# Kernel tuning notes

Hardware: AMD Instinct MI355X
Metric: run time of the kernel (lower is better)

Reference implementation:

```python
import jax, jax.numpy as jnp
import numpy as np

N, E, F_IN, H = 50000, 800000, 500, 96

def setup_inputs() -> dict:
    key = jax.random.key(0)
    ks = jax.random.split(key, 10)
    x = jax.random.normal(ks[0], (N, F_IN), dtype=jnp.float32)
    src = jax.random.randint(ks[1], (E,), 0, N, dtype=jnp.int32)
    dst = jax.random.randint(ks[2], (E,), 0, N, dtype=jnp.int32)
    perm = jax.random.permutation(ks[3], N).astype(jnp.int32)
    W1 = jax.random.normal(ks[4], (F_IN, H), dtype=jnp.float32) / np.sqrt(F_IN)
    b1 = jnp.zeros((H,), jnp.float32)
    a1 = jnp.full((H,), 0.25, jnp.float32)  # PReLU init
    W2 = jax.random.normal(ks[5], (H, H), dtype=jnp.float32) / np.sqrt(H)
    b2 = jnp.zeros((H,), jnp.float32)
    a2 = jnp.full((H,), 0.25, jnp.float32)
    Wm = jax.random.normal(ks[6], (H, H), dtype=jnp.float32) / np.sqrt(H)
    bm = jnp.zeros((H,), jnp.float32)
    return {"x": x, "src": src, "dst": dst, "perm": perm,
            "W1": W1, "b1": b1, "a1": a1, "W2": W2, "b2": b2, "a2": a2,
            "Wm": Wm, "bm": bm}

def reference(x, src, dst, perm, W1, b1, a1, W2, b2, a2, Wm, bm):
    n = x.shape[0]
    ones = jnp.ones_like(src, dtype=x.dtype)
    deg_out = jnp.clip(jax.ops.segment_sum(ones, src, num_segments=n), 1.0)
    deg_in = jnp.clip(jax.ops.segment_sum(ones, dst, num_segments=n), 1.0)
    norm_out = (deg_out ** -0.5)[:, None]  # [N,1]
    norm_in = (deg_in ** -0.5)[:, None]

    def gconv(h, W, b, a):
        # DGL GraphConv, norm='both': D_out^-1/2 -> W -> A -> D_in^-1/2 -> +b -> PReLU
        h = (h * norm_out) @ W                                  # [N,H]
        agg = jax.ops.segment_sum(h[src], dst, num_segments=n)  # SpMM via gather/scatter
        h = agg * norm_in + b
        return jnp.where(h >= 0, h, a * h)                      # PReLU

    def encode(feat):
        h = gconv(feat, W1, b1, a1)
        return gconv(h, W2, b2, a2)

    z1 = encode(x)
    z2 = encode(x[perm])  # corrupted view: permuted node features
    z1 = z1 @ Wm + bm
    z2 = z2 @ Wm + bm
    return jnp.concatenate([z1.sum(1), z2.sum(1)], axis=0)  # [2N]
```

## Files before the change

### kernel.cpp

```cpp
#include <hip/hip_runtime.h>

#define H96 96

typedef __attribute__((ext_vector_type(8))) short bf16x8_t;
typedef __attribute__((ext_vector_type(4))) float f32x4_t;
typedef __attribute__((ext_vector_type(8))) _Float16 half8_t;

__global__ void deg8_kernel(const int* __restrict__ src, const int* __restrict__ dst,
                            int* __restrict__ d8, int E, int NP8) {
    int e = blockIdx.x * blockDim.x + threadIdx.x;
    int c = blockIdx.x & 7;
    if (e < E) {
        int* base = d8 + (size_t)c * 2 * NP8;
        atomicAdd(base + src[e], 1);
        atomicAdd(base + NP8 + dst[e], 1);
    }
}

__global__ void degred_kernel(const int* __restrict__ d8, const int* __restrict__ perm,
                              int* __restrict__ deg_in, int* __restrict__ iperm,
                              float* __restrict__ no, float* __restrict__ ni,
                              int N, int NP8) {
    int i = blockIdx.x * 256 + threadIdx.x;
    if (i >= N) return;
    int so = 0, si = 0;
#pragma unroll
    for (int c = 0; c < 8; c++) {
        so += d8[(size_t)c * 2 * NP8 + i];
        si += d8[(size_t)c * 2 * NP8 + NP8 + i];
    }
    deg_in[i] = si;
    no[i] = rsqrtf(fmaxf((float)so, 1.0f));
    ni[i] = rsqrtf(fmaxf((float)si, 1.0f));
    iperm[perm[i]] = i;
}

__global__ void scanA_kernel(const int* __restrict__ in, int* __restrict__ pre,
                             int* __restrict__ bsums, int n) {
    __shared__ int s[256];
    int i = blockIdx.x * 256 + threadIdx.x;
    int v = (i < n) ? in[i] : 0;
    s[threadIdx.x] = v;
    __syncthreads();
    for (int off = 1; off < 256; off <<= 1) {
        int t = (threadIdx.x >= off) ? s[threadIdx.x - off] : 0;
        __syncthreads();
        s[threadIdx.x] += t;
        __syncthreads();
    }
    if (i < n) pre[i] = s[threadIdx.x] - v;
    if (threadIdx.x == 255) bsums[blockIdx.x] = s[255];
}

__global__ void scanB_kernel(int* __restrict__ bsums, int nb) {
    __shared__ int s[256];
    int v = (threadIdx.x < nb) ? bsums[threadIdx.x] : 0;
    s[threadIdx.x] = v;
    __syncthreads();
    for (int off = 1; off < 256; off <<= 1) {
        int t = (threadIdx.x >= off) ? s[threadIdx.x - off] : 0;
        __syncthreads();
        s[threadIdx.x] += t;
        __syncthreads();
    }
    if (threadIdx.x < nb) bsums[threadIdx.x] = s[threadIdx.x] - v;
}

__global__ void rowfin_kernel(const int* __restrict__ pre, const int* __restrict__ bsums,
                              int* __restrict__ row_start, int* __restrict__ cursor,
                              int N, int E) {
    int i = blockIdx.x * 256 + threadIdx.x;
    if (i < N) {
        int v = pre[i] + bsums[blockIdx.x];
        row_start[i] = v;
        cursor[i] = v;
    }
    if (i == 0) row_start[N] = E;
}

__global__ void scatter_kernel(const int* __restrict__ src, const int* __restrict__ dst,
                               const float* __restrict__ norm_out,
                               int* __restrict__ cursor, int2* __restrict__ edge2, int E) {
    int e = blockIdx.x * 256 + threadIdx.x;
    if (e < E) {
        int d = dst[e];
        int s = src[e];
        int p = atomicAdd(cursor + d, 1);
        edge2[p] = make_int2(s, __float_as_int(norm_out[s]));
    }
}

__global__ void histblk_kernel(const int* __restrict__ deg, int* __restrict__ hb,
                               int N, int nb) {
    __shared__ int h[256];
    h[threadIdx.x] = 0;
    __syncthreads();
    int i = blockIdx.x * 256 + threadIdx.x;
    if (i < N) atomicAdd(&h[min(deg[i], 255)], 1);
    __syncthreads();
    hb[threadIdx.x * nb + blockIdx.x] = h[threadIdx.x];
}

__global__ void place2_kernel(const int* __restrict__ deg, const int* __restrict__ hpre,
                              const int* __restrict__ bsums, int* __restrict__ order,
                              int N, int nb) {
    __shared__ int cur[256];
    int idx = threadIdx.x * nb + blockIdx.x;
    cur[threadIdx.x] = hpre[idx] + bsums[idx >> 8];
    __syncthreads();
    int i = blockIdx.x * 256 + threadIdx.x;
    if (i < N) {
        int b = min(deg[i], 255);
        int p = atomicAdd(&cur[b], 1);
        order[p] = i;
    }
}

__device__ __forceinline__ void f2bf2(float v, unsigned short& h, unsigned short& l) {
    unsigned int b = __float_as_uint(v);
    unsigned short hh = (unsigned short)((b + 0x7FFFu + ((b >> 16) & 1u)) >> 16);
    float fh = __uint_as_float(((unsigned int)hh) << 16);
    float r = v - fh;
    unsigned int rb = __float_as_uint(r);
    unsigned short ll = (unsigned short)((rb + 0x7FFFu + ((rb >> 16) & 1u)) >> 16);
    h = hh; l = ll;
}

__device__ __forceinline__ void cvt8(const float f[8], bf16x8_t& ah, bf16x8_t& al) {
    union { unsigned int u[4]; bf16x8_t v; } H, L;
#pragma unroll
    for (int i = 0; i < 4; i++) {
        float v0 = f[2 * i], v1 = f[2 * i + 1];
        unsigned int b0 = __float_as_uint(v0);
        unsigned int b1 = __float_as_uint(v1);
        unsigned int m0 = b0 & 0xFFFF0000u;
        unsigned int m1 = b1 & 0xFFFF0000u;
        float r0 = v0 - __uint_as_float(m0);
        float r1 = v1 - __uint_as_float(m1);
        H.u[i] = (b0 >> 16) | m1;
        L.u[i] = (__float_as_uint(r0) >> 16) | (__float_as_uint(r1) & 0xFFFF0000u);
    }
    ah = H.v; al = L.v;
}

__global__ void weights_prep(const float* __restrict__ W1, const float* __restrict__ W2,
                             const float* __restrict__ Wm, const float* __restrict__ bm,
                             unsigned short* __restrict__ w1h, unsigned short* __restrict__ w1l,
                             unsigned short* __restrict__ w2h, unsigned short* __restrict__ w2l,
                             float* __restrict__ wsum, float* __restrict__ bsum,
                             int F, int KP1) {
    int idx = blockIdx.x * 256 + threadIdx.x;
    int z1 = 96 * KP1, z2 = z1 + 96 * 96;
    if (idx < z1) {
        int n = idx / KP1, k = idx - n * KP1;
        float v = (k < F) ? W1[(size_t)k * 96 + n] : 0.f;
        unsigned short h, l;
        f2bf2(v, h, l);
        w1h[idx] = h; w1l[idx] = l;
    } else if (idx < z2) {
        int t = idx - z1;
        int n = t / 96, k = t - n * 96;
        float v = W2[(size_t)k * 96 + n];
        unsigned short h, l;
        f2bf2(v, h, l);
        w2h[t] = h; w2l[t] = l;
    } else if (idx < z2 + 96) {
        int c = idx - z2;
        float s = 0.f;
        for (int j = 0; j < 96; j++) s += Wm[c * 96 + j];
        wsum[c] = s;
    } else if (idx == z2 + 96) {
        float s = 0.f;
        for (int j = 0; j < 96; j++) s += bm[j];
        bsum[0] = s;
    }
}

#define GBM 64
#define GBK 32

__device__ __forceinline__ void gload_lds16(const void* g, void* l) {
    __builtin_amdgcn_global_load_lds(
        (const __attribute__((address_space(1))) unsigned int*)g,
        (__attribute__((address_space(3))) unsigned int*)l, 16, 0, 0);
}

__global__ __launch_bounds__(256, 6) void gemm_mfma(const void* __restrict__ Av,
                                                    const unsigned short* __restrict__ Bth,
                                                    const unsigned short* __restrict__ Btl,
                                                    _Float16* __restrict__ C16,
                                                    const int* __restrict__ ipermArr,
                                                    int M, int K, int KP) {
    __shared__ alignas(16) unsigned short Bs[2][2][96][4][8];
    int tid = threadIdx.x;
    int wid = tid >> 6, lane = tid & 63;
    int q = lane >> 4, mn = lane & 15;
    int row0 = blockIdx.x * GBM + wid * 16;
    int arow = min(row0 + mn, M - 1);
    int nk = (K + GBK - 1) / GBK;

    const float* A32 = (const float*)Av;

    const unsigned short* gsrc[3];
    int lbase[3];
#pragma unroll
    for (int i = 0; i < 3; i++) {
        int c = wid * 192 + i * 64 + lane;
        int part = (c >= 384) ? 1 : 0;
        int rem = c - part * 384;
        int row = rem >> 2, slot = rem & 3;
        int kc = slot ^ ((row >> 1) & 3);
        gsrc[i] = (part ? Btl : Bth) + (size_t)row * KP + kc * 8;
        lbase[i] = (wid * 192 + i * 64) * 8;
    }

    auto stage = [&](int t, int buf) {
#pragma unroll
        for (int i = 0; i < 3; i++)
            gload_lds16(gsrc[i] + (size_t)t * GBK, &Bs[buf][0][0][0][0] + lbase[i]);
    };

    auto loadA = [&](int t, float* f) {
        int gk = t * GBK + q * 8;
        if (gk + 8 <= K) {
            float4 v0 = *(const float4*)(A32 + (size_t)arow * K + gk);
            float4 v1 = *(const float4*)(A32 + (size_t)arow * K + gk + 4);
            f[0] = v0.x; f[1] = v0.y; f[2] = v0.z; f[3] = v0.w;
            f[4] = v1.x; f[5] = v1.y; f[6] = v1.z; f[7] = v1.w;
        } else {
#pragma unroll
            for (int c = 0; c < 8; c++)
                f[c] = (gk + c < K) ? A32[(size_t)arow * K + gk + c] : 0.f;
        }
    };

    f32x4_t acc[6] = {};
    float f[8], fn[8];

    stage(0, 0);
    loadA(0, f);

    int slotR = q ^ ((mn >> 1) & 3);

    for (int t = 0; t < nk; t++) {
        int tn = (t + 1 < nk) ? t + 1 : nk - 1;
        stage(tn, (t + 1) & 1);
        loadA(tn, fn);
        asm volatile("s_waitcnt vmcnt(5)" ::: "memory");
        __builtin_amdgcn_sched_barrier(0);
        __builtin_amdgcn_s_barrier();

        bf16x8_t ah, al;
        cvt8(f, ah, al);

        const unsigned short* bp = &Bs[t & 1][0][0][0][0] + mn * 32 + slotR * 8;
#pragma unroll
        for (int ct = 0; ct < 6; ct++) {
            bf16x8_t bh = *(const bf16x8_t*)(bp + ct * 512);
            bf16x8_t bl = *(const bf16x8_t*)(bp + 3072 + ct * 512);
            acc[ct] = __builtin_amdgcn_mfma_f32_16x16x32_bf16(ah, bh, acc[ct], 0, 0, 0);
            acc[ct] = __builtin_amdgcn_mfma_f32_16x16x32_bf16(ah, bl, acc[ct], 0, 0, 0);
            acc[ct] = __builtin_amdgcn_mfma_f32_16x16x32_bf16(al, bh, acc[ct], 0, 0, 0);
        }
        asm volatile("s_waitcnt lgkmcnt(0)" ::: "memory");
        __builtin_amdgcn_sched_barrier(0);
        __builtin_amdgcn_s_barrier();

#pragma unroll
        for (int c = 0; c < 8; c++) f[c] = fn[c];
    }

    asm volatile("s_waitcnt vmcnt(0)" ::: "memory");
    __builtin_amdgcn_sched_barrier(0);

#pragma unroll
    for (int reg = 0; reg < 4; reg++) {
        int gr = row0 + q * 4 + reg;
        if (gr < M) {
            int ip = ipermArr[gr];
#pragma unroll
            for (int ct = 0; ct < 6; ct++) {
                _Float16 v = (_Float16)acc[ct][reg];
                C16[(size_t)gr * 192 + ct * 16 + mn] = v;
                C16[(size_t)ip * 192 + 96 + ct * 16 + mn] = v;
            }
        }
    }
}

__global__ __launch_bounds__(256, 4) void gemm_small(const _Float16* __restrict__ A16,
                                                     const unsigned short* __restrict__ Bth,
                                                     const unsigned short* __restrict__ Btl,
                                                     _Float16* __restrict__ C16,
                                                     int M) {
    __shared__ alignas(16) unsigned short Bs[3][2][96][4][8];
    const int K = 96;
    int tid = threadIdx.x;
    int wid = tid >> 6, lane = tid & 63;
    int q = lane >> 4, mn = lane & 15;
    int row0 = blockIdx.x * GBM + wid * 16;
    int arow = min(row0 + mn, M - 1);

    const unsigned short* gsrc[3];
    int lbase[3];
#pragma unroll
    for (int i = 0; i < 3; i++) {
        int c = wid * 192 + i * 64 + lane;
        int part = (c >= 384) ? 1 : 0;
        int rem = c - part * 384;
        int row = rem >> 2, slot = rem & 3;
        int kc = slot ^ ((row >> 1) & 3);
        gsrc[i] = (part ? Btl : Bth) + (size_t)row * K + kc * 8;
        lbase[i] = (wid * 192 + i * 64) * 8;
    }

#pragma unroll
    for (int t = 0; t < 3; t++)
#pragma unroll
        for (int i = 0; i < 3; i++)
            gload_lds16(gsrc[i] + (size_t)t * GBK, &Bs[t][0][0][0][0] + lbase[i]);

    uint4 ra0 = *(const uint4*)(A16 + (size_t)arow * K + 0 * GBK + q * 8);
    uint4 ra1 = *(const uint4*)(A16 + (size_t)arow * K + 1 * GBK + q * 8);
    uint4 ra2 = *(const uint4*)(A16 + (size_t)arow * K + 2 * GBK + q * 8);

    asm volatile("s_waitcnt vmcnt(0)" ::: "memory");
    __builtin_amdgcn_sched_barrier(0);
    __builtin_amdgcn_s_barrier();

    f32x4_t acc[6] = {};
    int slotR = q ^ ((mn >> 1) & 3);

    auto step = [&](int t, const uint4& raw) {
        float f[8];
        const _Float16* hp = (const _Float16*)&raw;
#pragma unroll
        for (int c = 0; c < 8; c++) f[c] = (float)hp[c];
        bf16x8_t ah, al;
        cvt8(f, ah, al);
        const unsigned short* bp = &Bs[t][0][0][0][0] + mn * 32 + slotR * 8;
#pragma unroll
        for (int ct = 0; ct < 6; ct++) {
            bf16x8_t bh = *(const bf16x8_t*)(bp + ct * 512);
            bf16x8_t bl = *(const bf16x8_t*)(bp + 3072 + ct * 512);
            acc[ct] = __builtin_amdgcn_mfma_f32_16x16x32_bf16(ah, bh, acc[ct], 0, 0, 0);
            acc[ct] = __builtin_amdgcn_mfma_f32_16x16x32_bf16(ah, bl, acc[ct], 0, 0, 0);
            acc[ct] = __builtin_amdgcn_mfma_f32_16x16x32_bf16(al, bh, acc[ct], 0, 0, 0);
        }
    };

    step(0, ra0);
    step(1, ra1);
    step(2, ra2);

#pragma unroll
    for (int reg = 0; reg < 4; reg++) {
        int gr = row0 + q * 4 + reg;
        if (gr < M) {
#pragma unroll
            for (int ct = 0; ct < 6; ct++)
                C16[(size_t)gr * H96 + ct * 16 + mn] = (_Float16)acc[ct][reg];
        }
    }
}

__device__ __forceinline__ void fmah8(float4& a, float4& b, float s, half8_t v) {
    a.x = fmaf(s, (float)v[0], a.x); a.y = fmaf(s, (float)v[1], a.y);
    a.z = fmaf(s, (float)v[2], a.z); a.w = fmaf(s, (float)v[3], a.w);
    b.x = fmaf(s, (float)v[4], b.x); b.y = fmaf(s, (float)v[5], b.y);
    b.z = fmaf(s, (float)v[6], b.z); b.w = fmaf(s, (float)v[7], b.w);
}

__device__ __forceinline__ float4 prelu4(float4 acc, float ni, float4 b, float4 a) {
    float4 h;
    h.x = fmaf(acc.x, ni, b.x); h.x = (h.x >= 0.f) ? h.x : a.x * h.x;
    h.y = fmaf(acc.y, ni, b.y); h.y = (h.y >= 0.f) ? h.y : a.y * h.y;
    h.z = fmaf(acc.z, ni, b.z); h.z = (h.z >= 0.f) ? h.z : a.z * h.z;
    h.w = fmaf(acc.w, ni, b.w); h.w = (h.w >= 0.f) ? h.w : a.w * h.w;
    return h;
}

__global__ __launch_bounds__(384) void spmm1_dual(
        const half8_t* __restrict__ yp, const int* __restrict__ row_start,
        const int2* __restrict__ edge2, const int* __restrict__ order,
        const float* __restrict__ norm_out, const float* __restrict__ norm_in,
        const float* __restrict__ b1, const float* __restrict__ a1,
        half8_t* __restrict__ hpair, int N) {
    int g = blockIdx.x * 32 + threadIdx.y;
    if (g >= N) return;
    int d = order[g];
    int tx = threadIdx.x;
    int beg = row_start[d], end = row_start[d + 1];
    const half8_t* yt = yp + tx;
    float4 a1a = {0,0,0,0}, a1b = {0,0,0,0}, a2a = {0,0,0,0}, a2b = {0,0,0,0};
    int j = beg;
    for (; j + 8 <= end; j += 8) {
        int2 e[8];
#pragma unroll
        for (int q = 0; q < 8; q++) e[q] = edge2[j + q];
        half8_t u[8], w[8];
#pragma unroll
        for (int q = 0; q < 8; q++) u[q] = yt[(size_t)e[q].x * 24];
#pragma unroll
        for (int q = 0; q < 8; q++) w[q] = yt[(size_t)e[q].x * 24 + 12];
#pragma unroll
        for (int q = 0; q < 8; q++) {
            float n = __int_as_float(e[q].y);
            fmah8(a1a, a1b, n, u[q]);
            fmah8(a2a, a2b, n, w[q]);
        }
    }
    for (; j < end; j++) {
        int2 e = edge2[j];
        float n = __int_as_float(e.y);
        fmah8(a1a, a1b, n, yt[(size_t)e.x * 24]);
        fmah8(a2a, a2b, n, yt[(size_t)e.x * 24 + 12]);
    }
    float ni = norm_in[d], no = norm_out[d];
    float4 bb0 = ((const float4*)b1)[tx * 2], bb1 = ((const float4*)b1)[tx * 2 + 1];
    float4 aa0 = ((const float4*)a1)[tx * 2], aa1 = ((const float4*)a1)[tx * 2 + 1];
    float4 r1a = prelu4(a1a, ni, bb0, aa0), r1b = prelu4(a1b, ni, bb1, aa1);
    float4 r2a = prelu4(a2a, ni, bb0, aa0), r2b = prelu4(a2b, ni, bb1, aa1);
    half8_t o1, o2;
    o1[0] = (_Float16)(r1a.x * no); o1[1] = (_Float16)(r1a.y * no);
    o1[2] = (_Float16)(r1a.z * no); o1[3] = (_Float16)(r1a.w * no);
    o1[4] = (_Float16)(r1b.x * no); o1[5] = (_Float16)(r1b.y * no);
    o1[6] = (_Float16)(r1b.z * no); o1[7] = (_Float16)(r1b.w * no);
    o2[0] = (_Float16)(r2a.x * no); o2[1] = (_Float16)(r2a.y * no);
    o2[2] = (_Float16)(r2a.z * no); o2[3] = (_Float16)(r2a.w * no);
    o2[4] = (_Float16)(r2b.x * no); o2[5] = (_Float16)(r2b.y * no);
    o2[6] = (_Float16)(r2b.z * no); o2[7] = (_Float16)(r2b.w * no);
    hpair[(size_t)d * 24 + tx] = o1;
    hpair[(size_t)d * 24 + 12 + tx] = o2;
}

__global__ __launch_bounds__(384) void spmm2_dual(
        const half8_t* __restrict__ th,
        const int* __restrict__ row_start, const int2* __restrict__ edge2,
        const int* __restrict__ order, const float* __restrict__ norm_in,
        const float* __restrict__ b2, const float* __restrict__ a2,
        const float* __restrict__ wsum, const float* __restrict__ bsum,
        float* __restrict__ outp, int N) {
    int g = blockIdx.x * 32 + threadIdx.y;
    int tx = threadIdx.x;
    int ty = threadIdx.y;
    bool valid = (g < N);
    int d = valid ? order[g] : 0;
    int beg = 0, end = 0;
    if (valid) { beg = row_start[d]; end = row_start[d + 1]; }
    const half8_t* t1 = th + tx;
    float4 a1a = {0,0,0,0}, a1b = {0,0,0,0}, a2a = {0,0,0,0}, a2b = {0,0,0,0};
    int j = beg;
    for (; j + 8 <= end; j += 8) {
        int s[8];
#pragma unroll
        for (int q = 0; q < 8; q++) s[q] = edge2[j + q].x;
        half8_t u[8], w[8];
#pragma unroll
        for (int q = 0; q < 8; q++) u[q] = t1[(size_t)s[q] * 24];
#pragma unroll
        for (int q = 0; q < 8; q++) w[q] = t1[(size_t)s[q] * 24 + 12];
#pragma unroll
        for (int q = 0; q < 8; q++) {
            fmah8(a1a, a1b, 1.f, u[q]);
            fmah8(a2a, a2b, 1.f, w[q]);
        }
    }
    for (; j < end; j++) {
        int s = edge2[j].x;
        fmah8(a1a, a1b, 1.f, t1[(size_t)s * 24]);
        fmah8(a2a, a2b, 1.f, t1[(size_t)s * 24 + 12]);
    }
    float ni = valid ? norm_in[d] : 0.f;
    float4 bb0 = ((const float4*)b2)[tx * 2], bb1 = ((const float4*)b2)[tx * 2 + 1];
    float4 aa0 = ((const float4*)a2)[tx * 2], aa1 = ((const float4*)a2)[tx * 2 + 1];
    float4 wv0 = ((const float4*)wsum)[tx * 2], wv1 = ((const float4*)wsum)[tx * 2 + 1];
    float4 r1a = prelu4(a1a, ni, bb0, aa0), r1b = prelu4(a1b, ni, bb1, aa1);
    float4 r2a = prelu4(a2a, ni, bb0, aa0), r2b = prelu4(a2b, ni, bb1, aa1);
    float p1 = r1a.x * wv0.x + r1a.y * wv0.y + r1a.z * wv0.z + r1a.w * wv0.w
             + r1b.x * wv1.x + r1b.y * wv1.y + r1b.z * wv1.z + r1b.w * wv1.w;
    float p2 = r2a.x * wv0.x + r2a.y * wv0.y + r2a.z * wv0.z + r2a.w * wv0.w
             + r2b.x * wv1.x + r2b.y * wv1.y + r2b.z * wv1.z + r2b.w * wv1.w;
    __shared__ float red1[32][12];
    __shared__ float red2[32][12];
    red1[ty][tx] = p1;
    red2[ty][tx] = p2;
    __syncthreads();
    if (tx == 0 && valid) {
        float s1 = 0.f, s2 = 0.f;
#pragma unroll
        for (int k = 0; k < 12; k++) { s1 += red1[ty][k]; s2 += red2[ty][k]; }
        outp[d] = s1 + bsum[0];
        outp[N + d] = s2 + bsum[0];
    }
}

extern "C" void kernel_launch(void* const* d_in, const int* in_sizes, int n_in,
                              void* d_out, int out_size, void* d_ws, size_t ws_size,
                              hipStream_t stream) {
    const float* x    = (const float*)d_in[0];
    const int*   src  = (const int*)d_in[1];
    const int*   dst  = (const int*)d_in[2];
    const int*   perm = (const int*)d_in[3];
    const float* W1   = (const float*)d_in[4];
    const float* b1   = (const float*)d_in[5];
    const float* a1   = (const float*)d_in[6];
    const float* W2   = (const float*)d_in[7];
    const float* b2   = (const float*)d_in[8];
    const float* a2   = (const float*)d_in[9];
    const float* Wm   = (const float*)d_in[10];
    const float* bm   = (const float*)d_in[11];
    float* out = (float*)d_out;

    int E = in_sizes[1];
    int N = in_sizes[3];
    int F = in_sizes[0] / N;
    int KP1 = ((F + GBK - 1) / GBK) * GBK;

    size_t NP = ((size_t)N + 256) & ~(size_t)255;
    size_t EP = ((size_t)E + 255) & ~(size_t)255;
    int nb = (N + 255) / 256;
    size_t HB = ((size_t)256 * nb + 255) & ~(size_t)255;

    int* iperm     = (int*)d_ws;
    int* deg_in    = iperm + NP;
    int* pre       = deg_in + NP;
    int* row_start = pre + NP;
    int* cursor    = row_start + NP;
    int* order     = cursor + NP;
    int* bsums     = order + NP;
    int* hb        = bsums + 256;
    int* hpre      = hb + HB;
    int2* edge2    = (int2*)(hpre + HB);
    float* norm_out = (float*)(edge2 + EP);
    float* norm_in  = norm_out + NP;
    float* wsum     = norm_in + NP;
    float* bsum     = wsum + 128;
    unsigned short* w1th = (unsigned short*)(bsum + 128);
    unsigned short* w1tl = w1th + 49664;
    unsigned short* w2th = w1tl + 49664;
    unsigned short* w2tl = w2th + 9728;
    _Float16* fpA = (_Float16*)(w2tl + 9728);
    _Float16* fpB = fpA + ((size_t)N * 192 + 256);
    _Float16* ypair = fpA;
    _Float16* hpair = fpB;
    _Float16* th    = fpA;

    int* d8 = (int*)edge2;

    hipMemsetAsync(d8, 0, 16 * NP * sizeof(int), stream);
    deg8_kernel<<<(E + 255) / 256, 256, 0, stream>>>(src, dst, d8, E, (int)NP);
    degred_kernel<<<(N + 255) / 256, 256, 0, stream>>>(d8, perm, deg_in, iperm,
                                                       norm_out, norm_in, N, (int)NP);

    scanA_kernel<<<nb, 256, 0, stream>>>(deg_in, pre, bsums, N);
    scanB_kernel<<<1, 256, 0, stream>>>(bsums, nb);
    rowfin_kernel<<<nb, 256, 0, stream>>>(pre, bsums, row_start, cursor, N, E);
    scatter_kernel<<<(E + 255) / 256, 256, 0, stream>>>(src, dst, norm_out, cursor,
                                                        edge2, E);

    histblk_kernel<<<nb, 256, 0, stream>>>(deg_in, hb, N, nb);
    int n2 = 256 * nb;
    int nb2 = (n2 + 255) / 256;
    scanA_kernel<<<nb2, 256, 0, stream>>>(hb, hpre, bsums, n2);
    scanB_kernel<<<1, 256, 0, stream>>>(bsums, nb2);
    place2_kernel<<<nb, 256, 0, stream>>>(deg_in, hpre, bsums, order, N, nb);

    int wtot = 96 * KP1 + 96 * 96 + 96 + 1;
    weights_prep<<<(wtot + 255) / 256, 256, 0, stream>>>(W1, W2, Wm, bm, w1th, w1tl,
                                                         w2th, w2tl, wsum, bsum, F, KP1);

    gemm_mfma<<<(N + GBM - 1) / GBM, 256, 0, stream>>>(x, w1th, w1tl, ypair, iperm,
                                                       N, F, KP1);

    int nsb = (N + 31) / 32;
    spmm1_dual<<<nsb, dim3(12, 32), 0, stream>>>(
        (const half8_t*)ypair, row_start, edge2, order, norm_out, norm_in,
        b1, a1, (half8_t*)hpair, N);

    gemm_small<<<(2 * N + GBM - 1) / GBM, 256, 0, stream>>>(hpair, w2th, w2tl, th, 2 * N);

    spmm2_dual<<<nsb, dim3(12, 32), 0, stream>>>(
        (const half8_t*)th, row_start, edge2, order, norm_in, b2, a2,
        wsum, bsum, out, N);
}
```

Baseline: 434.6 us.

## Replace global-atomic degree counting with LDS range-partitioned histograms

Degree counting moves from global atomics into 8 privatized copies to a kernel that splits the node range into 8 slices and the edge list into 64 chunks. Each block builds an LDS histogram of its slice from a vectorized scan of its edge chunk and writes 16-bit partial counts. The reduction kernel then sums the 64 partials per node. This removes the memset and the global atomic traffic, but every edge is now read 8 times, and LDS use is about 50KB per block, which limits occupancy.

```diff
diff --git a/kernel.cpp b/kernel.cpp
--- a/kernel.cpp
+++ b/kernel.cpp
@@ -6,28 +6,68 @@
 typedef __attribute__((ext_vector_type(4))) float f32x4_t;
 typedef __attribute__((ext_vector_type(8))) _Float16 half8_t;
 
-__global__ void deg8_kernel(const int* __restrict__ src, const int* __restrict__ dst,
-                            int* __restrict__ d8, int E, int NP8) {
-    int e = blockIdx.x * blockDim.x + threadIdx.x;
-    int c = blockIdx.x & 7;
-    if (e < E) {
-        int* base = d8 + (size_t)c * 2 * NP8;
-        atomicAdd(base + src[e], 1);
-        atomicAdd(base + NP8 + dst[e], 1);
-    }
-}
-
-__global__ void degred_kernel(const int* __restrict__ d8, const int* __restrict__ perm,
+#define NRANGE 8
+#define NCHUNK 64
+
+__global__ __launch_bounds__(256) void hist2_kernel(const int* __restrict__ src,
+                                                    const int* __restrict__ dst,
+                                                    unsigned short* __restrict__ parts,
+                                                    int E, int RS, int ecpc) {
+    extern __shared__ int h[];
+    int r = blockIdx.x >> 6;
+    int c = blockIdx.x & 63;
+    int lo = r * RS;
+    for (int i = threadIdx.x; i < 2 * RS; i += 256) h[i] = 0;
+    __syncthreads();
+    int e0 = c * ecpc;
+    int e1 = min(e0 + ecpc, E);
+    for (int base = e0 + threadIdx.x * 4; base < e1; base += 1024) {
+        int cnt = min(4, e1 - base);
+        if (cnt == 4) {
+            int4 sv = *(const int4*)(src + base);
+            int4 dv = *(const int4*)(dst + base);
+            int a;
+            a = sv.x - lo; if ((unsigned)a < (unsigned)RS) atomicAdd(&h[a], 1);
+            a = sv.y - lo; if ((unsigned)a < (unsigned)RS) atomicAdd(&h[a], 1);
+            a = sv.z - lo; if ((unsigned)a < (unsigned)RS) atomicAdd(&h[a], 1);
+            a = sv.w - lo; if ((unsigned)a < (unsigned)RS) atomicAdd(&h[a], 1);
+            a = dv.x - lo; if ((unsigned)a < (unsigned)RS) atomicAdd(&h[RS + a], 1);
+            a = dv.y - lo; if ((unsigned)a < (unsigned)RS) atomicAdd(&h[RS + a], 1);
+            a = dv.z - lo; if ((unsigned)a < (unsigned)RS) atomicAdd(&h[RS + a], 1);
+            a = dv.w - lo; if ((unsigned)a < (unsigned)RS) atomicAdd(&h[RS + a], 1);
+        } else {
+            for (int k = 0; k < cnt; k++) {
+                int a = src[base + k] - lo;
+                if ((unsigned)a < (unsigned)RS) atomicAdd(&h[a], 1);
+                a = dst[base + k] - lo;
+                if ((unsigned)a < (unsigned)RS) atomicAdd(&h[RS + a], 1);
+            }
+        }
+    }
+    __syncthreads();
+    unsigned short* po = parts + ((size_t)(r * 2 + 0) * NCHUNK + c) * RS;
+    unsigned short* pi = parts + ((size_t)(r * 2 + 1) * NCHUNK + c) * RS;
+    for (int i = threadIdx.x; i < RS; i += 256) {
+        po[i] = (unsigned short)h[i];
+        pi[i] = (unsigned short)h[RS + i];
+    }
+}
+
+__global__ void degred_kernel(const unsigned short* __restrict__ parts,
+                              const int* __restrict__ perm,
                               int* __restrict__ deg_in, int* __restrict__ iperm,
                               float* __restrict__ no, float* __restrict__ ni,
-                              int N, int NP8) {
+                              int N, int RS) {
     int i = blockIdx.x * 256 + threadIdx.x;
     if (i >= N) return;
+    int r = i / RS, idx = i - r * RS;
+    const unsigned short* po = parts + ((size_t)(r * 2 + 0) * NCHUNK) * RS + idx;
+    const unsigned short* pi = parts + ((size_t)(r * 2 + 1) * NCHUNK) * RS + idx;
     int so = 0, si = 0;
 #pragma unroll
-    for (int c = 0; c < 8; c++) {
-        so += d8[(size_t)c * 2 * NP8 + i];
-        si += d8[(size_t)c * 2 * NP8 + NP8 + i];
+    for (int c = 0; c < NCHUNK; c++) {
+        so += po[(size_t)c * RS];
+        si += pi[(size_t)c * RS];
     }
     deg_in[i] = si;
     no[i] = rsqrtf(fmaxf((float)so, 1.0f));
@@ -546,12 +586,14 @@
     _Float16* hpair = fpB;
     _Float16* th    = fpA;
 
-    int* d8 = (int*)edge2;
-
-    hipMemsetAsync(d8, 0, 16 * NP * sizeof(int), stream);
-    deg8_kernel<<<(E + 255) / 256, 256, 0, stream>>>(src, dst, d8, E, (int)NP);
-    degred_kernel<<<(N + 255) / 256, 256, 0, stream>>>(d8, perm, deg_in, iperm,
-                                                       norm_out, norm_in, N, (int)NP);
+    unsigned short* parts = (unsigned short*)fpA;
+
+    int RS = (N + NRANGE - 1) / NRANGE;
+    int ecpc = ((E + NCHUNK - 1) / NCHUNK + 3) & ~3;
+    hist2_kernel<<<NRANGE * NCHUNK, 256, 2 * RS * (int)sizeof(int), stream>>>(
+        src, dst, parts, E, RS, ecpc);
+    degred_kernel<<<(N + 255) / 256, 256, 0, stream>>>(parts, perm, deg_in, iperm,
+                                                       norm_out, norm_in, N, RS);
 
     scanA_kernel<<<nb, 256, 0, stream>>>(deg_in, pre, bsums, N);
     scanB_kernel<<<1, 256, 0, stream>>>(bsums, nb);
```

Measured after the change: 389.1 us. 10.5% less time.
